# Kernel optimization log

Measured on AMD Instinct MI355X. Metric: run time of the kernel, lower is better.

Reference implementation:

```python
import jax, jax.numpy as jnp
import numpy as np

N_ATOMS = 300000
MAX_NBR = 12
AFL = 64      # atom_fea_len
NFL = 41      # nbr_fea_len
NCONV = 3
HFL = 128     # h_fea_len


def setup_inputs() -> dict:
    key = jax.random.key(0)
    ks = jax.random.split(key, 24)
    def w(k, shape, fan_in):
        return jax.random.normal(k, shape, dtype=jnp.float32) / np.sqrt(fan_in)
    return {
        "atom_fea": jax.random.normal(ks[0], (N_ATOMS, 92), dtype=jnp.float32),
        "nbr_fea": jax.random.normal(ks[1], (N_ATOMS, MAX_NBR, NFL), dtype=jnp.float32),
        "nbr_fea_idx": jax.random.randint(ks[2], (N_ATOMS, MAX_NBR), 0, N_ATOMS),
        "ae_w": w(ks[3], (92, AFL), 92), "ae_b": jnp.zeros((AFL,), jnp.float32),
        "ne_w": w(ks[4], (NFL, AFL), NFL), "ne_b": jnp.zeros((AFL,), jnp.float32),
        "msg_w1": w(ks[5], (NCONV, 2 * AFL, AFL), 2 * AFL), "msg_b1": jnp.zeros((NCONV, AFL), jnp.float32),
        "msg_w2": w(ks[6], (NCONV, AFL, AFL), AFL), "msg_b2": jnp.zeros((NCONV, AFL), jnp.float32),
        "upd_w1": w(ks[7], (NCONV, 2 * AFL, AFL), 2 * AFL), "upd_b1": jnp.zeros((NCONV, AFL), jnp.float32),
        "upd_w2": w(ks[8], (NCONV, AFL, AFL), AFL), "upd_b2": jnp.zeros((NCONV, AFL), jnp.float32),
        "fx_w1": w(ks[9], (AFL, HFL), AFL), "fx_b1": jnp.zeros((HFL,), jnp.float32),
        "fx_w2": w(ks[10], (HFL, HFL // 2), HFL), "fx_b2": jnp.zeros((HFL // 2,), jnp.float32),
        "prop_w": w(ks[11], (4, HFL // 2), HFL // 2), "prop_b": jnp.zeros((4,), jnp.float32),
    }


def _forward(atom_fea, nbr_fea, nbr_fea_idx,
             ae_w, ae_b, ne_w, ne_b,
             msg_w1, msg_b1, msg_w2, msg_b2,
             upd_w1, upd_b1, upd_w2, upd_b2,
             fx_w1, fx_b1, fx_w2, fx_b2, prop_w, prop_b):
    relu = jax.nn.relu
    a = atom_fea @ ae_w + ae_b                      # [N, 64] atom embedding
    _nbr_emb = nbr_fea @ ne_w + ne_b                # [N, K, 64] (computed but unused by conv layers, as in source)
    for l in range(NCONV):
        nb = a[nbr_fea_idx]                         # gather: [N, K, 64]
        self_exp = jnp.broadcast_to(a[:, None, :], nb.shape)
        comb = jnp.concatenate([self_exp, nb], axis=-1)   # [N, K, 128]
        m = relu(comb @ msg_w1[l] + msg_b1[l]) @ msg_w2[l] + msg_b2[l]  # [N, K, 64]
        agg = jnp.sum(m, axis=1)                    # sum-aggregate over neighbors: [N, 64]
        u_in = jnp.concatenate([a, agg], axis=-1)   # [N, 128]
        upd = relu(u_in @ upd_w1[l] + upd_b1[l]) @ upd_w2[l] + upd_b2[l]
        a = relu(a + upd)                           # residual + ReLU
    raw = a
    # feature extractor (Dropout in eval mode = identity)
    af = relu(a @ fx_w1 + fx_b1) @ fx_w2 + fx_b2    # [N, 64]
    props = jnp.einsum('nh,ph->np', af, prop_w) + prop_b  # [N, 4]: bond_strength, local_charge, coordination_energy, migration_barrier
    return props, af, raw


def reference(atom_fea, nbr_fea, nbr_fea_idx,
              ae_w, ae_b, ne_w, ne_b,
              msg_w1, msg_b1, msg_w2, msg_b2,
              upd_w1, upd_b1, upd_w2, upd_b2,
              fx_w1, fx_b1, fx_w2, fx_b2, prop_w, prop_b):
    return _forward(atom_fea, nbr_fea, nbr_fea_idx,
                    ae_w, ae_b, ne_w, ne_b,
                    msg_w1, msg_b1, msg_w2, msg_b2,
                    upd_w1, upd_b1, upd_w2, upd_b2,
                    fx_w1, fx_b1, fx_w2, fx_b2, prop_w, prop_b)
```

## Files before the change

kernel.cpp:

```cpp
#include <hip/hip_runtime.h>
#include <hip/hip_bf16.h>


constexpr int NA = 300000;

typedef short  s16x8 __attribute__((ext_vector_type(8)));
typedef float  f32x4 __attribute__((ext_vector_type(4)));

#define DEVFN static __device__ __forceinline__

DEVFN unsigned short f2bf(float x) {
  unsigned u = __float_as_uint(x);
  u += 0x7fffu + ((u >> 16) & 1u);
  return (unsigned short)(u >> 16);
}
DEVFN float bf2f(unsigned short h) { return __uint_as_float(((unsigned)h) << 16); }

DEVFN void mk_frag(const float* v, s16x8& hi, s16x8& lo) {
#pragma unroll
  for (int i = 0; i < 8; i += 2) {
    __hip_bfloat162 h2 = __float22bfloat162_rn(make_float2(v[i], v[i + 1]));
    float2 hf = __bfloat1622float2(h2);
    __hip_bfloat162 l2 = __float22bfloat162_rn(make_float2(v[i] - hf.x, v[i + 1] - hf.y));
    hi[i]     = (short)__bfloat16_as_ushort(h2.x);
    hi[i + 1] = (short)__bfloat16_as_ushort(h2.y);
    lo[i]     = (short)__bfloat16_as_ushort(l2.x);
    lo[i + 1] = (short)__bfloat16_as_ushort(l2.y);
  }
}

DEVFN f32x4 mf3(s16x8 ah, s16x8 al, s16x8 bh, s16x8 bl, f32x4 c) {
  c = __builtin_amdgcn_mfma_f32_16x16x32_bf16(al, bh, c, 0, 0, 0);
  c = __builtin_amdgcn_mfma_f32_16x16x32_bf16(ah, bl, c, 0, 0, 0);
  c = __builtin_amdgcn_mfma_f32_16x16x32_bf16(ah, bh, c, 0, 0, 0);
  return c;
}

DEVFN void ldB(const unsigned short* __restrict__ WH, const unsigned short* __restrict__ WL,
               int seg, int kt, int ct, int CT, int l, s16x8& bh, s16x8& bl) {
  size_t o = (size_t)seg + ((size_t)((kt * CT + ct) * 64 + l)) * 8;
  bh = *(const s16x8*)(WH + o);
  bl = *(const s16x8*)(WL + o);
}

DEVFN f32x4 bias4(float bv) { f32x4 c; c[0] = bv; c[1] = bv; c[2] = bv; c[3] = bv; return c; }

DEVFN void stage_mm(const unsigned short* __restrict__ WH,
                    const unsigned short* __restrict__ WL,
                    int seg, int kt0,
                    const s16x8 (&fh)[4][2], const s16x8 (&fl)[4][2],
                    int l, f32x4 (&cc)[4][4]) {
#pragma unroll
  for (int ct = 0; ct < 4; ++ct)
#pragma unroll
    for (int kt = 0; kt < 2; ++kt) {
      s16x8 bh, bl; ldB(WH, WL, seg, kt0 + kt, ct, 4, l, bh, bl);
#pragma unroll
      for (int gr = 0; gr < 4; ++gr)
        cc[gr][ct] = mf3(fh[gr][kt], fl[gr][kt], bh, bl, cc[gr][ct]);
    }
}

DEVFN void put_half(float (*sl)[69], int m, int g, const f32x4 (&cc)[4][4], int h) {
#pragma unroll
  for (int gr = 0; gr < 4; ++gr)
#pragma unroll
    for (int c = 0; c < 2; ++c)
#pragma unroll
      for (int r = 0; r < 4; ++r)
        sl[16 * c + m][gr * 17 + 4 * g + r] = cc[gr][2 * h + c][r];
}
DEVFN void get_half(const float (*sl)[69], int m, int g, int gr, float* v) {
#pragma unroll
  for (int i = 0; i < 8; ++i) v[i] = sl[8 * g + i][gr * 17 + m];
}

DEVFN void trans_frags(float (*sl)[69], int m, int g, const f32x4 (&cc)[4][4],
                       s16x8 (&fh)[4][2], s16x8 (&fl)[4][2]) {
#pragma unroll
  for (int h = 0; h < 2; ++h) {
    put_half(sl, m, g, cc, h);
#pragma unroll
    for (int gr = 0; gr < 4; ++gr) {
      float v[8];
      get_half(sl, m, g, gr, v);
      mk_frag(v, fh[gr][h], fl[gr][h]);
    }
  }
}

DEVFN void trans_store_bf(float (*sl)[69], int m, int g, const f32x4 (&cc)[4][4],
                          unsigned short* __restrict__ B, const int (&nat)[4], const bool (&ok)[4]) {
#pragma unroll
  for (int h = 0; h < 2; ++h) {
    put_half(sl, m, g, cc, h);
#pragma unroll
    for (int gr = 0; gr < 4; ++gr) {
      float v[8];
      get_half(sl, m, g, gr, v);
      if (ok[gr]) {
        uint4 q;
        unsigned* qp = (unsigned*)&q;
#pragma unroll
        for (int p = 0; p < 4; ++p)
          qp[p] = (unsigned)f2bf(v[2 * p]) | ((unsigned)f2bf(v[2 * p + 1]) << 16);
        *(uint4*)(B + (size_t)nat[gr] * 64 + 32 * h + 8 * g) = q;
      }
    }
  }
}

__global__ __launch_bounds__(256) void k_prep(
    const float* __restrict__ ae, const float* __restrict__ mw1,
    const float* __restrict__ mw2, const float* __restrict__ uw1,
    const float* __restrict__ uw2, const float* __restrict__ fx1,
    const float* __restrict__ fx2,
    unsigned short* __restrict__ WH, unsigned short* __restrict__ WL) {
  int e = blockIdx.x * 256 + threadIdx.x;
  const float* src;
  int K, N, loc;
  if (e < 6144) { src = ae; K = 92; N = 64; loc = e; }
  else if (e < 79872) {
    int r = e - 6144;
    int lyr = r / 24576, q = r % 24576;
    size_t l64 = (size_t)lyr * 64;
    if (q < 8192)       { src = mw1 + l64 * 128; K = 128; N = 64; loc = q; }
    else if (q < 12288) { src = mw2 + l64 * 64;  K = 64;  N = 64; loc = q - 8192; }
    else if (q < 20480) { src = uw1 + l64 * 128; K = 128; N = 64; loc = q - 12288; }
    else                { src = uw2 + l64 * 64;  K = 64;  N = 64; loc = q - 20480; }
  }
  else if (e < 88064) { src = fx1; K = 64;  N = 128; loc = e - 79872; }
  else if (e < 96256) { src = fx2; K = 128; N = 64;  loc = e - 88064; }
  else return;
  int k = (N == 64) ? (loc >> 6) : (loc >> 7);
  int j = loc & (N - 1);
  float v = (k < K) ? src[(size_t)k * N + j] : 0.f;
  unsigned short h = f2bf(v);
  int CT = N >> 4;
  int lane = ((k >> 3) & 3) * 16 + (j & 15);
  int fidx = (e - loc) + (((k >> 5) * CT + (j >> 4)) * 64 + lane) * 8 + (k & 7);
  WH[fidx] = h;
  WL[fidx] = f2bf(v - bf2f(h));
}

__global__ __launch_bounds__(256, 2) void k_embed_st(
    const float* __restrict__ X,
    const unsigned short* __restrict__ WH, const unsigned short* __restrict__ WL,
    const float* __restrict__ aeb, const float* __restrict__ b1,
    float* __restrict__ A0, unsigned short* __restrict__ S, unsigned short* __restrict__ T) {
  __shared__ float slab[4][32][69];
  int w = threadIdx.x >> 6, l = threadIdx.x & 63, m = l & 15, g = l >> 4;
  float (*sl)[69] = slab[w];
  int nbase = blockIdx.x * 256 + w * 64;
  int nat[4]; bool ok[4];
#pragma unroll
  for (int gr = 0; gr < 4; ++gr) {
    nat[gr] = nbase + gr * 16 + m;
    ok[gr] = nat[gr] < NA;
    if (!ok[gr]) nat[gr] = NA - 1;
  }

  f32x4 ca[4][4];
#pragma unroll
  for (int gr = 0; gr < 4; ++gr)
#pragma unroll
    for (int ct = 0; ct < 4; ++ct) ca[gr][ct] = bias4(aeb[16 * ct + m]);
#pragma unroll
  for (int kt = 0; kt < 3; ++kt) {
    s16x8 xh[4], xl[4];
#pragma unroll
    for (int gr = 0; gr < 4; ++gr) {
      const float* xr = X + (size_t)nat[gr] * 92;
      float v[8];
      if (kt < 2) {
        f32x4 a = *(const f32x4*)(xr + kt * 32 + g * 8);
        f32x4 b = *(const f32x4*)(xr + kt * 32 + g * 8 + 4);
        v[0]=a[0]; v[1]=a[1]; v[2]=a[2]; v[3]=a[3]; v[4]=b[0]; v[5]=b[1]; v[6]=b[2]; v[7]=b[3];
      } else if (g < 3) {
        f32x4 a = *(const f32x4*)(xr + 64 + g * 8);
        f32x4 b = *(const f32x4*)(xr + 64 + g * 8 + 4);
        v[0]=a[0]; v[1]=a[1]; v[2]=a[2]; v[3]=a[3]; v[4]=b[0]; v[5]=b[1]; v[6]=b[2]; v[7]=b[3];
      } else {
        f32x4 a = *(const f32x4*)(xr + 88);
        v[0]=a[0]; v[1]=a[1]; v[2]=a[2]; v[3]=a[3]; v[4]=0.f; v[5]=0.f; v[6]=0.f; v[7]=0.f;
      }
      mk_frag(v, xh[gr], xl[gr]);
    }
#pragma unroll
    for (int ct = 0; ct < 4; ++ct) {
      s16x8 bh, bl; ldB(WH, WL, 0, kt, ct, 4, l, bh, bl);
#pragma unroll
      for (int gr = 0; gr < 4; ++gr)
        ca[gr][ct] = mf3(xh[gr], xl[gr], bh, bl, ca[gr][ct]);
    }
  }

  s16x8 ah[4][2], al[4][2];
#pragma unroll
  for (int h = 0; h < 2; ++h) {
    put_half(sl, m, g, ca, h);
#pragma unroll
    for (int gr = 0; gr < 4; ++gr) {
      float v[8];
      get_half(sl, m, g, gr, v);
      if (ok[gr]) {
        float* p = A0 + (size_t)nat[gr] * 64 + 32 * h + 8 * g;
        *(float4*)p = make_float4(v[0], v[1], v[2], v[3]);
        *(float4*)(p + 4) = make_float4(v[4], v[5], v[6], v[7]);
      }
      mk_frag(v, ah[gr][h], al[gr][h]);
    }
  }

  f32x4 cs[4][4];
#pragma unroll
  for (int gr = 0; gr < 4; ++gr)
#pragma unroll
    for (int ct = 0; ct < 4; ++ct) cs[gr][ct] = bias4(b1[16 * ct + m]);
  stage_mm(WH, WL, 6144, 0, ah, al, l, cs);
  trans_store_bf(sl, m, g, cs, S, nat, ok);

  f32x4 cT[4][4];
#pragma unroll
  for (int gr = 0; gr < 4; ++gr)
#pragma unroll
    for (int ct = 0; ct < 4; ++ct) cT[gr][ct] = bias4(0.f);
  stage_mm(WH, WL, 6144, 2, ah, al, l, cT);
  trans_store_bf(sl, m, g, cT, T, nat, ok);
}

template <int HAS_NEXT, int HAS_FX>
__global__ __launch_bounds__(256, 2) void k_dense(
    const float* __restrict__ A, const unsigned short* __restrict__ S,
    const unsigned short* __restrict__ T, const int* __restrict__ IDX,
    const unsigned short* __restrict__ WH, const unsigned short* __restrict__ WL,
    int segW2, int segU1, int segU2, int segWn,
    const float* __restrict__ b2, const float* __restrict__ ub1,
    const float* __restrict__ ub2, const float* __restrict__ bn,
    const float* __restrict__ fb1, const float* __restrict__ fb2,
    const float* __restrict__ PW, const float* __restrict__ PB,
    float* __restrict__ Anew, unsigned short* __restrict__ Sout,
    unsigned short* __restrict__ Tout,
    float* __restrict__ AF, float* __restrict__ PR) {
  __shared__ float slab[4][32][69];
  int w = threadIdx.x >> 6, l = threadIdx.x & 63, m = l & 15, g = l >> 4;
  float (*sl)[69] = slab[w];
  int nbase = blockIdx.x * 256 + w * 64;
  int nat[4]; bool ok[4];
#pragma unroll
  for (int gr = 0; gr < 4; ++gr) {
    nat[gr] = nbase + gr * 16 + m;
    ok[gr] = nat[gr] < NA;
    if (!ok[gr]) nat[gr] = NA - 1;
  }

  s16x8 hh[4][2], hl[4][2];
#pragma unroll
  for (int gr = 0; gr < 4; ++gr) {
    const int* ip = IDX + (size_t)nat[gr] * 12;
    int4 i0 = *(const int4*)ip;
    int4 i1 = *(const int4*)(ip + 4);
    int4 i2 = *(const int4*)(ip + 8);
    int idxs[12] = {i0.x, i0.y, i0.z, i0.w, i1.x, i1.y, i1.z, i1.w,
                    i2.x, i2.y, i2.z, i2.w};
#pragma unroll
    for (int kt = 0; kt < 2; ++kt) {
      int f0 = 32 * kt + 8 * g;
      uint4 sv4 = *(const uint4*)(S + (size_t)nat[gr] * 64 + f0);
      float sv[8] = {
        bf2f((unsigned short)(sv4.x & 0xffff)), bf2f((unsigned short)(sv4.x >> 16)),
        bf2f((unsigned short)(sv4.y & 0xffff)), bf2f((unsigned short)(sv4.y >> 16)),
        bf2f((unsigned short)(sv4.z & 0xffff)), bf2f((unsigned short)(sv4.z >> 16)),
        bf2f((unsigned short)(sv4.w & 0xffff)), bf2f((unsigned short)(sv4.w >> 16))};
      float ha[8] = {0, 0, 0, 0, 0, 0, 0, 0};
#pragma unroll
      for (int c = 0; c < 12; ++c) {
        uint4 tv = *(const uint4*)(T + (size_t)idxs[c] * 64 + f0);
        ha[0] += fmaxf(sv[0] + bf2f((unsigned short)(tv.x & 0xffff)), 0.f);
        ha[1] += fmaxf(sv[1] + bf2f((unsigned short)(tv.x >> 16)), 0.f);
        ha[2] += fmaxf(sv[2] + bf2f((unsigned short)(tv.y & 0xffff)), 0.f);
        ha[3] += fmaxf(sv[3] + bf2f((unsigned short)(tv.y >> 16)), 0.f);
        ha[4] += fmaxf(sv[4] + bf2f((unsigned short)(tv.z & 0xffff)), 0.f);
        ha[5] += fmaxf(sv[5] + bf2f((unsigned short)(tv.z >> 16)), 0.f);
        ha[6] += fmaxf(sv[6] + bf2f((unsigned short)(tv.w & 0xffff)), 0.f);
        ha[7] += fmaxf(sv[7] + bf2f((unsigned short)(tv.w >> 16)), 0.f);
      }
      mk_frag(ha, hh[gr][kt], hl[gr][kt]);
    }
  }

  f32x4 cg[4][4];
#pragma unroll
  for (int gr = 0; gr < 4; ++gr)
#pragma unroll
    for (int ct = 0; ct < 4; ++ct) cg[gr][ct] = bias4(12.f * b2[16 * ct + m]);
  stage_mm(WH, WL, segW2, 0, hh, hl, l, cg);

  f32x4 cu[4][4];
#pragma unroll
  for (int gr = 0; gr < 4; ++gr)
#pragma unroll
    for (int ct = 0; ct < 4; ++ct) cu[gr][ct] = bias4(ub1[16 * ct + m]);
  {
    s16x8 arh[4][2], arl[4][2];
#pragma unroll
    for (int gr = 0; gr < 4; ++gr)
#pragma unroll
      for (int kt = 0; kt < 2; ++kt) {
        const float* p8 = A + (size_t)nat[gr] * 64 + kt * 32 + g * 8;
        f32x4 a = *(const f32x4*)p8;
        f32x4 b = *(const f32x4*)(p8 + 4);
        float v[8] = {a[0], a[1], a[2], a[3], b[0], b[1], b[2], b[3]};
        mk_frag(v, arh[gr][kt], arl[gr][kt]);
      }
    stage_mm(WH, WL, segU1, 0, arh, arl, l, cu);
  }
  {
    s16x8 qh[4][2], ql[4][2];
    trans_frags(sl, m, g, cg, qh, ql);
    stage_mm(WH, WL, segU1, 2, qh, ql, l, cu);
  }
#pragma unroll
  for (int gr = 0; gr < 4; ++gr)
#pragma unroll
    for (int ct = 0; ct < 4; ++ct)
#pragma unroll
      for (int r = 0; r < 4; ++r) cu[gr][ct][r] = fmaxf(cu[gr][ct][r], 0.f);

  f32x4 cd[4][4];
#pragma unroll
  for (int gr = 0; gr < 4; ++gr)
#pragma unroll
    for (int ct = 0; ct < 4; ++ct) cd[gr][ct] = bias4(ub2[16 * ct + m]);
  {
    s16x8 uh[4][2], ul[4][2];
    trans_frags(sl, m, g, cu, uh, ul);
    stage_mm(WH, WL, segU2, 0, uh, ul, l, cd);
  }

  s16x8 anh[4][2], anl[4][2];
#pragma unroll
  for (int h = 0; h < 2; ++h) {
    put_half(sl, m, g, cd, h);
#pragma unroll
    for (int gr = 0; gr < 4; ++gr) {
      float v[8];
      get_half(sl, m, g, gr, v);
      const float* ap = A + (size_t)nat[gr] * 64 + 32 * h + 8 * g;
      f32x4 a0 = *(const f32x4*)ap;
      f32x4 a1 = *(const f32x4*)(ap + 4);
#pragma unroll
      for (int i = 0; i < 4; ++i) {
        v[i]     = fmaxf(v[i] + a0[i], 0.f);
        v[i + 4] = fmaxf(v[i + 4] + a1[i], 0.f);
      }
      if (ok[gr]) {
        float* p = Anew + (size_t)nat[gr] * 64 + 32 * h + 8 * g;
        *(float4*)p = make_float4(v[0], v[1], v[2], v[3]);
        *(float4*)(p + 4) = make_float4(v[4], v[5], v[6], v[7]);
      }
      if constexpr (HAS_NEXT || HAS_FX) mk_frag(v, anh[gr][h], anl[gr][h]);
    }
  }

  if constexpr (HAS_NEXT) {
    f32x4 cs[4][4];
#pragma unroll
    for (int gr = 0; gr < 4; ++gr)
#pragma unroll
      for (int ct = 0; ct < 4; ++ct) cs[gr][ct] = bias4(bn[16 * ct + m]);
    stage_mm(WH, WL, segWn, 0, anh, anl, l, cs);
    trans_store_bf(sl, m, g, cs, Sout, nat, ok);

    f32x4 cT[4][4];
#pragma unroll
    for (int gr = 0; gr < 4; ++gr)
#pragma unroll
      for (int ct = 0; ct < 4; ++ct) cT[gr][ct] = bias4(0.f);
    stage_mm(WH, WL, segWn, 2, anh, anl, l, cT);
    trans_store_bf(sl, m, g, cT, Tout, nat, ok);
  }

  if constexpr (HAS_FX) {
    f32x4 cf[4][4];
#pragma unroll
    for (int gr = 0; gr < 4; ++gr)
#pragma unroll
      for (int ct = 0; ct < 4; ++ct) cf[gr][ct] = bias4(fb2[16 * ct + m]);

#pragma unroll
    for (int hr = 0; hr < 2; ++hr) {
      f32x4 chh[4][4];
#pragma unroll
      for (int gr = 0; gr < 4; ++gr)
#pragma unroll
        for (int ct = 0; ct < 4; ++ct)
          chh[gr][ct] = bias4(fb1[16 * (4 * hr + ct) + m]);
#pragma unroll
      for (int ct = 0; ct < 4; ++ct)
#pragma unroll
        for (int kt = 0; kt < 2; ++kt) {
          s16x8 bh, bl; ldB(WH, WL, 79872, kt, 4 * hr + ct, 8, l, bh, bl);
#pragma unroll
          for (int gr = 0; gr < 4; ++gr)
            chh[gr][ct] = mf3(anh[gr][kt], anl[gr][kt], bh, bl, chh[gr][ct]);
        }
#pragma unroll
      for (int gr = 0; gr < 4; ++gr)
#pragma unroll
        for (int ct = 0; ct < 4; ++ct)
#pragma unroll
          for (int r = 0; r < 4; ++r) chh[gr][ct][r] = fmaxf(chh[gr][ct][r], 0.f);

      s16x8 hfh[4][2], hfl[4][2];
      trans_frags(sl, m, g, chh, hfh, hfl);
      stage_mm(WH, WL, 88064, 2 * hr, hfh, hfl, l, cf);
    }

    float pp[4][4];
#pragma unroll
    for (int gr = 0; gr < 4; ++gr)
#pragma unroll
      for (int p = 0; p < 4; ++p) pp[gr][p] = 0.f;
#pragma unroll
    for (int h = 0; h < 2; ++h) {
      put_half(sl, m, g, cf, h);
      f32x4 pw0[4], pw1[4];
#pragma unroll
      for (int p = 0; p < 4; ++p) {
        const float* q = PW + p * 64 + 32 * h + 8 * g;
        pw0[p] = *(const f32x4*)q;
        pw1[p] = *(const f32x4*)(q + 4);
      }
#pragma unroll
      for (int gr = 0; gr < 4; ++gr) {
        float v[8];
        get_half(sl, m, g, gr, v);
        if (ok[gr]) {
          float* p = AF + (size_t)nat[gr] * 64 + 32 * h + 8 * g;
          *(float4*)p = make_float4(v[0], v[1], v[2], v[3]);
          *(float4*)(p + 4) = make_float4(v[4], v[5], v[6], v[7]);
        }
#pragma unroll
        for (int p = 0; p < 4; ++p)
#pragma unroll
          for (int i = 0; i < 4; ++i)
            pp[gr][p] += v[i] * pw0[p][i] + v[i + 4] * pw1[p][i];
      }
    }
#pragma unroll
    for (int gr = 0; gr < 4; ++gr) {
      float r0 = pp[gr][0], r1 = pp[gr][1], r2 = pp[gr][2], r3 = pp[gr][3];
      r0 += __shfl_xor(r0, 16); r0 += __shfl_xor(r0, 32);
      r1 += __shfl_xor(r1, 16); r1 += __shfl_xor(r1, 32);
      r2 += __shfl_xor(r2, 16); r2 += __shfl_xor(r2, 32);
      r3 += __shfl_xor(r3, 16); r3 += __shfl_xor(r3, 32);
      float sel = (g == 0) ? r0 : (g == 1) ? r1 : (g == 2) ? r2 : r3;
      if (ok[gr]) PR[(size_t)nat[gr] * 4 + g] = sel + PB[g];
    }
  }
}

extern "C" void kernel_launch(void* const* d_in, const int* in_sizes, int n_in,
                              void* d_out, int out_size, void* d_ws, size_t ws_size,
                              hipStream_t stream) {
  const float* atom_fea = (const float*)d_in[0];
  const int*   nbr_idx  = (const int*)d_in[2];
  const float* ae_w   = (const float*)d_in[3];
  const float* ae_b   = (const float*)d_in[4];
  const float* msg_w1 = (const float*)d_in[7];
  const float* msg_b1 = (const float*)d_in[8];
  const float* msg_w2 = (const float*)d_in[9];
  const float* msg_b2 = (const float*)d_in[10];
  const float* upd_w1 = (const float*)d_in[11];
  const float* upd_b1 = (const float*)d_in[12];
  const float* upd_w2 = (const float*)d_in[13];
  const float* upd_b2 = (const float*)d_in[14];
  const float* fx_w1  = (const float*)d_in[15];
  const float* fx_b1  = (const float*)d_in[16];
  const float* fx_w2  = (const float*)d_in[17];
  const float* fx_b2  = (const float*)d_in[18];
  const float* prop_w = (const float*)d_in[19];
  const float* prop_b = (const float*)d_in[20];

  float* props   = (float*)d_out;
  float* af_reg  = props + (size_t)NA * 4;
  float* raw_reg = af_reg + (size_t)NA * 64;
  unsigned short* S0 = (unsigned short*)d_ws;
  unsigned short* S1 = S0 + (size_t)NA * 64;
  unsigned short* T0 = S1 + (size_t)NA * 64;
  unsigned short* T1 = T0 + (size_t)NA * 64;
  unsigned short* WHp = T1 + (size_t)NA * 64;
  unsigned short* WLp = WHp + 96256;

  k_prep<<<376, 256, 0, stream>>>(ae_w, msg_w1, msg_w2, upd_w1, upd_w2,
                                  fx_w1, fx_w2, WHp, WLp);

  int ngrid = (NA + 255) / 256;
  k_embed_st<<<ngrid, 256, 0, stream>>>(atom_fea, WHp, WLp, ae_b, msg_b1,
                                        af_reg, S0, T0);

  const int base0 = 6144, base1 = 6144 + 24576, base2 = 6144 + 2 * 24576;

  k_dense<1, 0><<<ngrid, 256, 0, stream>>>(
      af_reg, S0, T0, nbr_idx, WHp, WLp,
      base0 + 8192, base0 + 12288, base0 + 20480, base1,
      msg_b2, upd_b1, upd_b2, msg_b1 + 64,
      fx_b1, fx_b2, prop_w, prop_b,
      raw_reg, S1, T1, nullptr, nullptr);

  k_dense<1, 0><<<ngrid, 256, 0, stream>>>(
      raw_reg, S1, T1, nbr_idx, WHp, WLp,
      base1 + 8192, base1 + 12288, base1 + 20480, base2,
      msg_b2 + 64, upd_b1 + 64, upd_b2 + 64, msg_b1 + 128,
      fx_b1, fx_b2, prop_w, prop_b,
      af_reg, S0, T0, nullptr, nullptr);

  k_dense<0, 1><<<ngrid, 256, 0, stream>>>(
      af_reg, S0, T0, nbr_idx, WHp, WLp,
      base2 + 8192, base2 + 12288, base2 + 20480, 0,
      msg_b2 + 128, upd_b1 + 128, upd_b2 + 128, msg_b1,
      fx_b1, fx_b2, prop_w, prop_b,
      raw_reg, S1, T1, af_reg, props);
}
```

Measured before the change: 630.2 us.

## Store intermediate atom features in bf16 and update S/A buffers in place

```diff
diff --git a/kernel.cpp b/kernel.cpp
--- a/kernel.cpp
+++ b/kernel.cpp
@@ -36,6 +36,12 @@
   return c;
 }
 
+DEVFN f32x4 mf2(s16x8 ah, s16x8 bh, s16x8 bl, f32x4 c) {
+  c = __builtin_amdgcn_mfma_f32_16x16x32_bf16(ah, bl, c, 0, 0, 0);
+  c = __builtin_amdgcn_mfma_f32_16x16x32_bf16(ah, bh, c, 0, 0, 0);
+  return c;
+}
+
 DEVFN void ldB(const unsigned short* __restrict__ WH, const unsigned short* __restrict__ WL,
                int seg, int kt, int ct, int CT, int l, s16x8& bh, s16x8& bl) {
   size_t o = (size_t)seg + ((size_t)((kt * CT + ct) * 64 + l)) * 8;
@@ -61,6 +67,22 @@
     }
 }
 
+DEVFN void stage_mm2(const unsigned short* __restrict__ WH,
+                     const unsigned short* __restrict__ WL,
+                     int seg, int kt0,
+                     const s16x8 (&fh)[4][2],
+                     int l, f32x4 (&cc)[4][4]) {
+#pragma unroll
+  for (int ct = 0; ct < 4; ++ct)
+#pragma unroll
+    for (int kt = 0; kt < 2; ++kt) {
+      s16x8 bh, bl; ldB(WH, WL, seg, kt0 + kt, ct, 4, l, bh, bl);
+#pragma unroll
+      for (int gr = 0; gr < 4; ++gr)
+        cc[gr][ct] = mf2(fh[gr][kt], bh, bl, cc[gr][ct]);
+    }
+}
+
 DEVFN void put_half(float (*sl)[69], int m, int g, const f32x4 (&cc)[4][4], int h) {
 #pragma unroll
   for (int gr = 0; gr < 4; ++gr)
@@ -89,6 +111,15 @@
   }
 }
 
+DEVFN void pack_store8(unsigned short* __restrict__ p, const float* v) {
+  uint4 q;
+  unsigned* qp = (unsigned*)&q;
+#pragma unroll
+  for (int i = 0; i < 4; ++i)
+    qp[i] = (unsigned)f2bf(v[2 * i]) | ((unsigned)f2bf(v[2 * i + 1]) << 16);
+  *(uint4*)p = q;
+}
+
 DEVFN void trans_store_bf(float (*sl)[69], int m, int g, const f32x4 (&cc)[4][4],
                           unsigned short* __restrict__ B, const int (&nat)[4], const bool (&ok)[4]) {
 #pragma unroll
@@ -98,14 +129,7 @@
     for (int gr = 0; gr < 4; ++gr) {
       float v[8];
       get_half(sl, m, g, gr, v);
-      if (ok[gr]) {
-        uint4 q;
-        unsigned* qp = (unsigned*)&q;
-#pragma unroll
-        for (int p = 0; p < 4; ++p)
-          qp[p] = (unsigned)f2bf(v[2 * p]) | ((unsigned)f2bf(v[2 * p + 1]) << 16);
-        *(uint4*)(B + (size_t)nat[gr] * 64 + 32 * h + 8 * g) = q;
-      }
+      if (ok[gr]) pack_store8(B + (size_t)nat[gr] * 64 + 32 * h + 8 * g, v);
     }
   }
 }
@@ -147,7 +171,8 @@
     const float* __restrict__ X,
     const unsigned short* __restrict__ WH, const unsigned short* __restrict__ WL,
     const float* __restrict__ aeb, const float* __restrict__ b1,
-    float* __restrict__ A0, unsigned short* __restrict__ S, unsigned short* __restrict__ T) {
+    unsigned short* __restrict__ A, unsigned short* __restrict__ S,
+    unsigned short* __restrict__ T) {
   __shared__ float slab[4][32][69];
   int w = threadIdx.x >> 6, l = threadIdx.x & 63, m = l & 15, g = l >> 4;
   float (*sl)[69] = slab[w];
@@ -203,11 +228,7 @@
     for (int gr = 0; gr < 4; ++gr) {
       float v[8];
       get_half(sl, m, g, gr, v);
-      if (ok[gr]) {
-        float* p = A0 + (size_t)nat[gr] * 64 + 32 * h + 8 * g;
-        *(float4*)p = make_float4(v[0], v[1], v[2], v[3]);
-        *(float4*)(p + 4) = make_float4(v[4], v[5], v[6], v[7]);
-      }
+      if (ok[gr]) pack_store8(A + (size_t)nat[gr] * 64 + 32 * h + 8 * g, v);
       mk_frag(v, ah[gr][h], al[gr][h]);
     }
   }
@@ -231,7 +252,7 @@
 
 template <int HAS_NEXT, int HAS_FX>
 __global__ __launch_bounds__(256, 2) void k_dense(
-    const float* __restrict__ A, const unsigned short* __restrict__ S,
+    unsigned short* __restrict__ A, unsigned short* __restrict__ S,
     const unsigned short* __restrict__ T, const int* __restrict__ IDX,
     const unsigned short* __restrict__ WH, const unsigned short* __restrict__ WL,
     int segW2, int segU1, int segU2, int segWn,
@@ -239,9 +260,8 @@
     const float* __restrict__ ub2, const float* __restrict__ bn,
     const float* __restrict__ fb1, const float* __restrict__ fb2,
     const float* __restrict__ PW, const float* __restrict__ PB,
-    float* __restrict__ Anew, unsigned short* __restrict__ Sout,
     unsigned short* __restrict__ Tout,
-    float* __restrict__ AF, float* __restrict__ PR) {
+    float* __restrict__ RawOut, float* __restrict__ AF, float* __restrict__ PR) {
   __shared__ float slab[4][32][69];
   int w = threadIdx.x >> 6, l = threadIdx.x & 63, m = l & 15, g = l >> 4;
   float (*sl)[69] = slab[w];
@@ -302,18 +322,13 @@
 #pragma unroll
     for (int ct = 0; ct < 4; ++ct) cu[gr][ct] = bias4(ub1[16 * ct + m]);
   {
-    s16x8 arh[4][2], arl[4][2];
+    s16x8 arh[4][2];
 #pragma unroll
     for (int gr = 0; gr < 4; ++gr)
 #pragma unroll
-      for (int kt = 0; kt < 2; ++kt) {
-        const float* p8 = A + (size_t)nat[gr] * 64 + kt * 32 + g * 8;
-        f32x4 a = *(const f32x4*)p8;
-        f32x4 b = *(const f32x4*)(p8 + 4);
-        float v[8] = {a[0], a[1], a[2], a[3], b[0], b[1], b[2], b[3]};
-        mk_frag(v, arh[gr][kt], arl[gr][kt]);
-      }
-    stage_mm(WH, WL, segU1, 0, arh, arl, l, cu);
+      for (int kt = 0; kt < 2; ++kt)
+        arh[gr][kt] = *(const s16x8*)(A + (size_t)nat[gr] * 64 + kt * 32 + g * 8);
+    stage_mm2(WH, WL, segU1, 0, arh, l, cu);
   }
   {
     s16x8 qh[4][2], ql[4][2];
@@ -346,18 +361,22 @@
     for (int gr = 0; gr < 4; ++gr) {
       float v[8];
       get_half(sl, m, g, gr, v);
-      const float* ap = A + (size_t)nat[gr] * 64 + 32 * h + 8 * g;
-      f32x4 a0 = *(const f32x4*)ap;
-      f32x4 a1 = *(const f32x4*)(ap + 4);
-#pragma unroll
-      for (int i = 0; i < 4; ++i) {
-        v[i]     = fmaxf(v[i] + a0[i], 0.f);
-        v[i + 4] = fmaxf(v[i + 4] + a1[i], 0.f);
-      }
-      if (ok[gr]) {
-        float* p = Anew + (size_t)nat[gr] * 64 + 32 * h + 8 * g;
-        *(float4*)p = make_float4(v[0], v[1], v[2], v[3]);
-        *(float4*)(p + 4) = make_float4(v[4], v[5], v[6], v[7]);
+      uint4 au = *(const uint4*)(A + (size_t)nat[gr] * 64 + 32 * h + 8 * g);
+      float av[8] = {
+        bf2f((unsigned short)(au.x & 0xffff)), bf2f((unsigned short)(au.x >> 16)),
+        bf2f((unsigned short)(au.y & 0xffff)), bf2f((unsigned short)(au.y >> 16)),
+        bf2f((unsigned short)(au.z & 0xffff)), bf2f((unsigned short)(au.z >> 16)),
+        bf2f((unsigned short)(au.w & 0xffff)), bf2f((unsigned short)(au.w >> 16))};
+#pragma unroll
+      for (int i = 0; i < 8; ++i) v[i] = fmaxf(v[i] + av[i], 0.f);
+      if constexpr (HAS_FX) {
+        if (ok[gr]) {
+          float* p = RawOut + (size_t)nat[gr] * 64 + 32 * h + 8 * g;
+          *(float4*)p = make_float4(v[0], v[1], v[2], v[3]);
+          *(float4*)(p + 4) = make_float4(v[4], v[5], v[6], v[7]);
+        }
+      } else {
+        if (ok[gr]) pack_store8(A + (size_t)nat[gr] * 64 + 32 * h + 8 * g, v);
       }
       if constexpr (HAS_NEXT || HAS_FX) mk_frag(v, anh[gr][h], anl[gr][h]);
     }
@@ -370,7 +389,7 @@
 #pragma unroll
       for (int ct = 0; ct < 4; ++ct) cs[gr][ct] = bias4(bn[16 * ct + m]);
     stage_mm(WH, WL, segWn, 0, anh, anl, l, cs);
-    trans_store_bf(sl, m, g, cs, Sout, nat, ok);
+    trans_store_bf(sl, m, g, cs, S, nat, ok);
 
     f32x4 cT[4][4];
 #pragma unroll
@@ -486,10 +505,10 @@
   float* props   = (float*)d_out;
   float* af_reg  = props + (size_t)NA * 4;
   float* raw_reg = af_reg + (size_t)NA * 64;
-  unsigned short* S0 = (unsigned short*)d_ws;
-  unsigned short* S1 = S0 + (size_t)NA * 64;
-  unsigned short* T0 = S1 + (size_t)NA * 64;
-  unsigned short* T1 = T0 + (size_t)NA * 64;
+  unsigned short* Abf = (unsigned short*)d_ws;
+  unsigned short* S   = Abf + (size_t)NA * 64;
+  unsigned short* T0  = S + (size_t)NA * 64;
+  unsigned short* T1  = T0 + (size_t)NA * 64;
   unsigned short* WHp = T1 + (size_t)NA * 64;
   unsigned short* WLp = WHp + 96256;
 
@@ -498,28 +517,28 @@
 
   int ngrid = (NA + 255) / 256;
   k_embed_st<<<ngrid, 256, 0, stream>>>(atom_fea, WHp, WLp, ae_b, msg_b1,
-                                        af_reg, S0, T0);
+                                        Abf, S, T0);
 
   const int base0 = 6144, base1 = 6144 + 24576, base2 = 6144 + 2 * 24576;
 
   k_dense<1, 0><<<ngrid, 256, 0, stream>>>(
-      af_reg, S0, T0, nbr_idx, WHp, WLp,
+      Abf, S, T0, nbr_idx, WHp, WLp,
       base0 + 8192, base0 + 12288, base0 + 20480, base1,
       msg_b2, upd_b1, upd_b2, msg_b1 + 64,
       fx_b1, fx_b2, prop_w, prop_b,
-      raw_reg, S1, T1, nullptr, nullptr);
+      T1, nullptr, nullptr, nullptr);
 
   k_dense<1, 0><<<ngrid, 256, 0, stream>>>(
-      raw_reg, S1, T1, nbr_idx, WHp, WLp,
+      Abf, S, T1, nbr_idx, WHp, WLp,
       base1 + 8192, base1 + 12288, base1 + 20480, base2,
       msg_b2 + 64, upd_b1 + 64, upd_b2 + 64, msg_b1 + 128,
       fx_b1, fx_b2, prop_w, prop_b,
-      af_reg, S0, T0, nullptr, nullptr);
+      T0, nullptr, nullptr, nullptr);
 
   k_dense<0, 1><<<ngrid, 256, 0, stream>>>(
-      af_reg, S0, T0, nbr_idx, WHp, WLp,
+      Abf, S, T0, nbr_idx, WHp, WLp,
       base2 + 8192, base2 + 12288, base2 + 20480, 0,
       msg_b2 + 128, upd_b1 + 128, upd_b2 + 128, msg_b1,
       fx_b1, fx_b2, prop_w, prop_b,
-      raw_reg, S1, T1, af_reg, props);
-}
+      T1, raw_reg, af_reg, props);
+}
```

After: 546.0 us. 1.15x faster.
